# Kernel tuning notes

Measured on AMD Instinct MI355X. Metric: run time of the kernel, lower is better.

The kernel has to match this reference:

```python
import jax, jax.numpy as jnp
import numpy as np

K = 100          # neighbours per slate item (self.k)
SLATE = 5        # slate_size
D = 20           # doc / proto embedding dim
N_DOCS = 2_000_000
NN_DIM = [256, 512, 100]  # last layer actually outputs SLATE*D = 100


def setup_inputs() -> dict:
    key = jax.random.key(0)
    ks = jax.random.split(key, 8)
    s = 0.05
    return {
        "input_state": jax.random.normal(ks[0], (D,), dtype=jnp.float32),
        "candidate_docs": jax.random.normal(ks[1], (N_DOCS, D), dtype=jnp.float32),
        "W0": jax.random.normal(ks[2], (D, NN_DIM[0]), dtype=jnp.float32) * s,
        "b0": jnp.zeros((NN_DIM[0],), dtype=jnp.float32),
        "W1": jax.random.normal(ks[3], (NN_DIM[0], NN_DIM[1]), dtype=jnp.float32) * s,
        "b1": jnp.zeros((NN_DIM[1],), dtype=jnp.float32),
        "W2": jax.random.normal(ks[4], (NN_DIM[1], SLATE * D), dtype=jnp.float32) * s,
        "b2": jnp.zeros((SLATE * D,), dtype=jnp.float32),
    }


def _proto_slate(x, W0, b0, W1, b1, W2, b2):
    # WolpertingerActorSlate.forward: leaky_relu after EVERY layer (torch default slope 0.01)
    x = jax.nn.leaky_relu(x @ W0 + b0)
    x = jax.nn.leaky_relu(x @ W1 + b1)
    x = jax.nn.leaky_relu(x @ W2 + b2)
    return x.reshape(SLATE, D)  # proto_action.view(slate_size, 20)


def reference(input_state, candidate_docs, W0, b0, W1, b1, W2, b2):
    proto = _proto_slate(input_state, W0, b0, W1, b1, W2, b2)  # [SLATE, D]
    # squared L2 distances via GEMM expansion (monotonic in L2 norm, so
    # top-k indices match torch.argsort(norm)[:k]); avoids [SLATE,N,D] blowup.
    cn2 = jnp.sum(candidate_docs * candidate_docs, axis=1)        # [N]
    pn2 = jnp.sum(proto * proto, axis=1)                          # [SLATE]
    d2 = cn2[None, :] - 2.0 * (proto @ candidate_docs.T) + pn2[:, None]  # [SLATE, N]
    # k smallest distances per slate item (fused selection instead of full argsort)
    _, idx = jax.lax.top_k(-d2, K)            # [SLATE, K]
    indices_tensor = idx.reshape(-1)          # [SLATE*K] (concat over slate positions)
    candidates_tensor = candidate_docs[indices_tensor]  # [SLATE*K, D]
    return candidates_tensor, indices_tensor
```

## Files before the change

kernel.cpp:

```cpp
#include <hip/hip_runtime.h>
#include <stdint.h>

#define N_DOCS 2000000
#define DIM 20
#define SLATE 5
#define KSEL 100
#define CUT_BIN 1544
#define CAPF 4096
#define BCAP 256
#define NT 256
#define NB 1024


__device__ __forceinline__ unsigned f2ord(float f) {
    unsigned u = __float_as_uint(f);
    return (u & 0x80000000u) ? ~u : (u | 0x80000000u);
}

__device__ __forceinline__ void load20(const float* __restrict__ base, float* v) {
    const float4* p = reinterpret_cast<const float4*>(base);
#pragma unroll
    for (int k = 0; k < 5; ++k) {
        float4 q = p[k];
        v[4*k+0] = q.x; v[4*k+1] = q.y; v[4*k+2] = q.z; v[4*k+3] = q.w;
    }
}

__global__ __launch_bounds__(512) void k_proto(
        const float* __restrict__ state,
        const float* __restrict__ W0, const float* __restrict__ b0,
        const float* __restrict__ W1, const float* __restrict__ b1,
        const float* __restrict__ W2, const float* __restrict__ b2,
        float* __restrict__ proto_g, float* __restrict__ pn2_g,
        unsigned* __restrict__ cnt) {
    __shared__ float s_x[DIM];
    __shared__ float s_h0[256];
    __shared__ float s_h1[512];
    __shared__ float s_p[SLATE*DIM];
    int t = threadIdx.x;
    if (t < 8) cnt[t] = 0u;
    if (t < DIM) s_x[t] = state[t];
    __syncthreads();
    if (t < 256) {
        float a = b0[t];
#pragma unroll
        for (int d = 0; d < DIM; ++d) a += s_x[d] * W0[d*256 + t];
        s_h0[t] = a > 0.f ? a : 0.01f*a;
    }
    __syncthreads();
    {
        float a = b1[t];
#pragma unroll 16
        for (int j = 0; j < 256; ++j) a += s_h0[j] * W1[j*512 + t];
        s_h1[t] = a > 0.f ? a : 0.01f*a;
    }
    __syncthreads();
    if (t < SLATE*DIM) {
        float a = b2[t];
#pragma unroll 16
        for (int j = 0; j < 512; ++j) a += s_h1[j] * W2[j*(SLATE*DIM) + t];
        float p = a > 0.f ? a : 0.01f*a;
        s_p[t] = p;
        proto_g[t] = p;
    }
    __syncthreads();
    if (t < SLATE) {
        float a = 0.f;
#pragma unroll
        for (int d = 0; d < DIM; ++d) { float p = s_p[t*DIM + d]; a += p*p; }
        pn2_g[t] = a;
    }
}

__global__ __launch_bounds__(NT) void k_pass1(
        const float* __restrict__ docs, const float* __restrict__ proto_g,
        const float* __restrict__ pn2_g,
        unsigned* __restrict__ cnt, uint2* __restrict__ cand, unsigned capN) {
    __shared__ float sp[SLATE*DIM];
    __shared__ float spn[SLATE];
    __shared__ uint2 buf[SLATE][BCAP];
    __shared__ unsigned bcnt[SLATE];
    __shared__ unsigned bbase[SLATE];
    int t = threadIdx.x;
    if (t < SLATE*DIM) sp[t] = proto_g[t];
    if (t < SLATE) { spn[t] = pn2_g[t]; bcnt[t] = 0u; }
    __syncthreads();
    const unsigned TOT = gridDim.x * blockDim.x;
    const unsigned gid = blockIdx.x * blockDim.x + t;
    for (unsigned base = 0; base < N_DOCS; base += 2u*TOT) {
        unsigned i0 = base + gid, i1 = base + gid + TOT;
        bool ok0 = i0 < N_DOCS, ok1 = i1 < N_DOCS;
        float a[DIM], b[DIM];
        load20(docs + (size_t)(ok0 ? i0 : 0u)*DIM, a);
        load20(docs + (size_t)(ok1 ? i1 : 0u)*DIM, b);
        float cn0 = 0.f, cn1 = 0.f;
#pragma unroll
        for (int d = 0; d < DIM; ++d) { cn0 += a[d]*a[d]; cn1 += b[d]*b[d]; }
#pragma unroll
        for (int s = 0; s < SLATE; ++s) {
            float d0 = 0.f, d1 = 0.f;
#pragma unroll
            for (int d = 0; d < DIM; ++d) {
                float p = sp[s*DIM + d];
                d0 += a[d]*p; d1 += b[d]*p;
            }
            float pn = spn[s];
            unsigned k0 = f2ord((cn0 - 2.f*d0) + pn);
            unsigned k1 = f2ord((cn1 - 2.f*d1) + pn);
            if (ok0 && (k0 >> 21) < CUT_BIN) {
                unsigned pos = atomicAdd(&bcnt[s], 1u);
                if (pos < BCAP) buf[s][pos] = make_uint2(k0, i0);
                else {
                    unsigned g = atomicAdd(&cnt[s], 1u);
                    if (g < capN) cand[(size_t)s*capN + g] = make_uint2(k0, i0);
                }
            }
            if (ok1 && (k1 >> 21) < CUT_BIN) {
                unsigned pos = atomicAdd(&bcnt[s], 1u);
                if (pos < BCAP) buf[s][pos] = make_uint2(k1, i1);
                else {
                    unsigned g = atomicAdd(&cnt[s], 1u);
                    if (g < capN) cand[(size_t)s*capN + g] = make_uint2(k1, i1);
                }
            }
        }
    }
    __syncthreads();
    if (t < SLATE) {
        unsigned m = bcnt[t]; if (m > BCAP) m = BCAP;
        bcnt[t] = m;
        bbase[t] = atomicAdd(&cnt[t], m);
    }
    __syncthreads();
#pragma unroll
    for (int s = 0; s < SLATE; ++s) {
        unsigned m = bcnt[s], base = bbase[s];
        for (unsigned j = t; j < m; j += NT) {
            unsigned g = base + j;
            if (g < capN) cand[(size_t)s*capN + g] = buf[s][j];
        }
    }
}

__global__ __launch_bounds__(256) void k_output(
        const unsigned* __restrict__ cnt, const uint2* __restrict__ cand,
        const float* __restrict__ docs, float* __restrict__ out, unsigned capN) {
    const int CH = (CUT_BIN + 7) / 8;
    int s = blockIdx.x;
    __shared__ unsigned sh[CUT_BIN];
    __shared__ unsigned part[(CUT_BIN + 7) / 8];
    __shared__ unsigned s_bstar, s_m;
    __shared__ unsigned fk[CAPF], fi[CAPF];
    int t = threadIdx.x;
    for (int b = t; b < CUT_BIN; b += 256) sh[b] = 0u;
    if (t == 0) s_m = 0;
    __syncthreads();
    unsigned M = cnt[s]; if (M > capN) M = capN;
    for (unsigned j = t; j < M; j += 256) {
        unsigned key = cand[(size_t)s*capN + j].x;
        atomicAdd(&sh[key >> 21], 1u);
    }
    __syncthreads();
    for (int c = t; c < CH; c += 256) {
        unsigned acc = 0;
#pragma unroll
        for (int j = 0; j < 8; ++j) {
            int b = c*8 + j;
            if (b < CUT_BIN) acc += sh[b];
        }
        part[c] = acc;
    }
    __syncthreads();
    if (t == 0) {
        unsigned cum = 0, bstar = CUT_BIN - 1;
        bool found = false;
        for (int c = 0; c < CH && !found; ++c) {
            if (cum + part[c] >= KSEL) {
                for (int j = 0; j < 8; ++j) {
                    int b = c*8 + j;
                    if (b >= CUT_BIN) break;
                    cum += sh[b];
                    if (cum >= KSEL) { bstar = b; found = true; break; }
                }
            } else cum += part[c];
        }
        s_bstar = bstar;
    }
    __syncthreads();
    unsigned bstar = s_bstar;
    for (unsigned j = t; j < M; j += 256) {
        uint2 c = cand[(size_t)s*capN + j];
        if ((c.x >> 21) <= bstar) {
            unsigned p = atomicAdd(&s_m, 1u);
            if (p < CAPF) { fk[p] = c.x; fi[p] = c.y; }
        }
    }
    __syncthreads();
    unsigned Mf = s_m < CAPF ? s_m : CAPF;
    for (unsigned j = t; j < Mf; j += 256) {
        unsigned kj = fk[j], ij = fi[j];
        unsigned r = 0;
        for (unsigned m = 0; m < Mf; ++m) {
            unsigned km = fk[m];
            r += (km < kj) || (km == kj && fi[m] < ij);
        }
        if (r < KSEL) {
            int row = s*KSEL + (int)r;
            out[(size_t)SLATE*KSEL*DIM + row] = (float)ij;
            const float* src = docs + (size_t)ij*DIM;
            float* dst = out + (size_t)row*DIM;
#pragma unroll
            for (int d = 0; d < DIM; ++d) dst[d] = src[d];
        }
    }
}

extern "C" void kernel_launch(void* const* d_in, const int* in_sizes, int n_in,
                              void* d_out, int out_size, void* d_ws, size_t ws_size,
                              hipStream_t stream) {
    const float* state = (const float*)d_in[0];
    const float* docs  = (const float*)d_in[1];
    const float* W0    = (const float*)d_in[2];
    const float* b0    = (const float*)d_in[3];
    const float* W1    = (const float*)d_in[4];
    const float* b1    = (const float*)d_in[5];
    const float* W2    = (const float*)d_in[6];
    const float* b2    = (const float*)d_in[7];
    float* out = (float*)d_out;

    char* ws = (char*)d_ws;
    float*    proto_g = (float*)(ws + 0);
    float*    pn2_g   = (float*)(ws + 512);
    unsigned* cnt     = (unsigned*)(ws + 1024);
    uint2*    cand    = (uint2*)(ws + 4096);

    size_t avail = ws_size > 4096 ? (ws_size - 4096) / (sizeof(uint2) * SLATE) : 0;
    unsigned capN = (unsigned)(avail < 32768 ? avail : 32768);

    k_proto<<<1, 512, 0, stream>>>(state, W0, b0, W1, b1, W2, b2,
                                   proto_g, pn2_g, cnt);
    k_pass1<<<NB, NT, 0, stream>>>(docs, proto_g, pn2_g, cnt, cand, capN);
    k_output<<<SLATE, 256, 0, stream>>>(cnt, cand, docs, out, capN);
}
```

Measured before the change: 356.6 us.

## Fuse output selection into pass1 via last-block-done pattern

Removes the separate k_output launch. The last block of k_pass1, found through an atomic counter in cnt[7] after a threadfence, now runs the per-slate histogram, threshold and rank selection for all five slate items one after another. The grid is doubled to 2048 blocks and CAPF is halved so the extra shared arrays fit in pass1's LDS. In exchange, the five-way parallel selection becomes serial in one block, and the larger static LDS footprint may lower pass1 occupancy.

```diff
diff --git a/kernel.cpp b/kernel.cpp
--- a/kernel.cpp
+++ b/kernel.cpp
@@ -6,10 +6,10 @@
 #define SLATE 5
 #define KSEL 100
 #define CUT_BIN 1544
-#define CAPF 4096
+#define CAPF 2048
 #define BCAP 256
 #define NT 256
-#define NB 1024
+#define NB 2048
 
 
 __device__ __forceinline__ unsigned f2ord(float f) {
@@ -75,12 +75,19 @@
 __global__ __launch_bounds__(NT) void k_pass1(
         const float* __restrict__ docs, const float* __restrict__ proto_g,
         const float* __restrict__ pn2_g,
-        unsigned* __restrict__ cnt, uint2* __restrict__ cand, unsigned capN) {
+        unsigned* __restrict__ cnt, uint2* __restrict__ cand, unsigned capN,
+        float* __restrict__ out) {
     __shared__ float sp[SLATE*DIM];
     __shared__ float spn[SLATE];
     __shared__ uint2 buf[SLATE][BCAP];
     __shared__ unsigned bcnt[SLATE];
     __shared__ unsigned bbase[SLATE];
+    __shared__ unsigned s_last;
+    __shared__ unsigned sh[CUT_BIN];
+    __shared__ unsigned part[(CUT_BIN + 7) / 8];
+    __shared__ unsigned s_bstar, s_m;
+    __shared__ unsigned fk[CAPF], fi[CAPF];
+
     int t = threadIdx.x;
     if (t < SLATE*DIM) sp[t] = proto_g[t];
     if (t < SLATE) { spn[t] = pn2_g[t]; bcnt[t] = 0u; }
@@ -140,78 +147,75 @@
             if (g < capN) cand[(size_t)s*capN + g] = buf[s][j];
         }
     }
-}
-
-__global__ __launch_bounds__(256) void k_output(
-        const unsigned* __restrict__ cnt, const uint2* __restrict__ cand,
-        const float* __restrict__ docs, float* __restrict__ out, unsigned capN) {
+    __threadfence();
+    __syncthreads();
+    if (t == 0) s_last = (atomicAdd(&cnt[7], 1u) == gridDim.x - 1u) ? 1u : 0u;
+    __syncthreads();
+    if (!s_last) return;
+    __threadfence();
+
     const int CH = (CUT_BIN + 7) / 8;
-    int s = blockIdx.x;
-    __shared__ unsigned sh[CUT_BIN];
-    __shared__ unsigned part[(CUT_BIN + 7) / 8];
-    __shared__ unsigned s_bstar, s_m;
-    __shared__ unsigned fk[CAPF], fi[CAPF];
-    int t = threadIdx.x;
-    for (int b = t; b < CUT_BIN; b += 256) sh[b] = 0u;
-    if (t == 0) s_m = 0;
-    __syncthreads();
-    unsigned M = cnt[s]; if (M > capN) M = capN;
-    for (unsigned j = t; j < M; j += 256) {
-        unsigned key = cand[(size_t)s*capN + j].x;
-        atomicAdd(&sh[key >> 21], 1u);
-    }
-    __syncthreads();
-    for (int c = t; c < CH; c += 256) {
-        unsigned acc = 0;
-#pragma unroll
-        for (int j = 0; j < 8; ++j) {
-            int b = c*8 + j;
-            if (b < CUT_BIN) acc += sh[b];
-        }
-        part[c] = acc;
-    }
-    __syncthreads();
-    if (t == 0) {
-        unsigned cum = 0, bstar = CUT_BIN - 1;
-        bool found = false;
-        for (int c = 0; c < CH && !found; ++c) {
-            if (cum + part[c] >= KSEL) {
-                for (int j = 0; j < 8; ++j) {
-                    int b = c*8 + j;
-                    if (b >= CUT_BIN) break;
-                    cum += sh[b];
-                    if (cum >= KSEL) { bstar = b; found = true; break; }
-                }
-            } else cum += part[c];
-        }
-        s_bstar = bstar;
-    }
-    __syncthreads();
-    unsigned bstar = s_bstar;
-    for (unsigned j = t; j < M; j += 256) {
-        uint2 c = cand[(size_t)s*capN + j];
-        if ((c.x >> 21) <= bstar) {
-            unsigned p = atomicAdd(&s_m, 1u);
-            if (p < CAPF) { fk[p] = c.x; fi[p] = c.y; }
-        }
-    }
-    __syncthreads();
-    unsigned Mf = s_m < CAPF ? s_m : CAPF;
-    for (unsigned j = t; j < Mf; j += 256) {
-        unsigned kj = fk[j], ij = fi[j];
-        unsigned r = 0;
-        for (unsigned m = 0; m < Mf; ++m) {
-            unsigned km = fk[m];
-            r += (km < kj) || (km == kj && fi[m] < ij);
-        }
-        if (r < KSEL) {
-            int row = s*KSEL + (int)r;
-            out[(size_t)SLATE*KSEL*DIM + row] = (float)ij;
-            const float* src = docs + (size_t)ij*DIM;
-            float* dst = out + (size_t)row*DIM;
-#pragma unroll
-            for (int d = 0; d < DIM; ++d) dst[d] = src[d];
-        }
+    for (int s = 0; s < SLATE; ++s) {
+        for (int b = t; b < CUT_BIN; b += NT) sh[b] = 0u;
+        if (t == 0) s_m = 0;
+        __syncthreads();
+        unsigned M = cnt[s]; if (M > capN) M = capN;
+        for (unsigned j = t; j < M; j += NT)
+            atomicAdd(&sh[cand[(size_t)s*capN + j].x >> 21], 1u);
+        __syncthreads();
+        for (int c = t; c < CH; c += NT) {
+            unsigned acc = 0;
+#pragma unroll
+            for (int j = 0; j < 8; ++j) {
+                int b = c*8 + j;
+                if (b < CUT_BIN) acc += sh[b];
+            }
+            part[c] = acc;
+        }
+        __syncthreads();
+        if (t == 0) {
+            unsigned cum = 0, bstar = CUT_BIN - 1;
+            bool found = false;
+            for (int c = 0; c < CH && !found; ++c) {
+                if (cum + part[c] >= KSEL) {
+                    for (int j = 0; j < 8; ++j) {
+                        int b = c*8 + j;
+                        if (b >= CUT_BIN) break;
+                        cum += sh[b];
+                        if (cum >= KSEL) { bstar = b; found = true; break; }
+                    }
+                } else cum += part[c];
+            }
+            s_bstar = bstar;
+        }
+        __syncthreads();
+        unsigned bstar = s_bstar;
+        for (unsigned j = t; j < M; j += NT) {
+            uint2 c = cand[(size_t)s*capN + j];
+            if ((c.x >> 21) <= bstar) {
+                unsigned p = atomicAdd(&s_m, 1u);
+                if (p < CAPF) { fk[p] = c.x; fi[p] = c.y; }
+            }
+        }
+        __syncthreads();
+        unsigned Mf = s_m < CAPF ? s_m : CAPF;
+        for (unsigned j = t; j < Mf; j += NT) {
+            unsigned kj = fk[j], ij = fi[j];
+            unsigned r = 0;
+            for (unsigned m = 0; m < Mf; ++m) {
+                unsigned km = fk[m];
+                r += (km < kj) || (km == kj && fi[m] < ij);
+            }
+            if (r < KSEL) {
+                int row = s*KSEL + (int)r;
+                out[(size_t)SLATE*KSEL*DIM + row] = (float)ij;
+                const float* src = docs + (size_t)ij*DIM;
+                float* dst = out + (size_t)row*DIM;
+#pragma unroll
+                for (int d = 0; d < DIM; ++d) dst[d] = src[d];
+            }
+        }
+        __syncthreads();
     }
 }
 
@@ -239,6 +243,5 @@
 
     k_proto<<<1, 512, 0, stream>>>(state, W0, b0, W1, b1, W2, b2,
                                    proto_g, pn2_g, cnt);
-    k_pass1<<<NB, NT, 0, stream>>>(docs, proto_g, pn2_g, cnt, cand, capN);
-    k_output<<<SLATE, 256, 0, stream>>>(cnt, cand, docs, out, capN);
-}
+    k_pass1<<<NB, NT, 0, stream>>>(docs, proto_g, pn2_g, cnt, cand, capN, out);
+}
```

Result: slower. 962.8 us (+170.0%).
